# Optimization experiments

Hardware: AMD Instinct MI355X
Metric: run time of the kernel (lower is better)

Reference implementation:

```python
import jax, jax.numpy as jnp
import numpy as np

IN_F, OUT_F, K = 1024, 1024, 12
EPS = 1e-6


def setup_inputs() -> dict:
    key = jax.random.key(0)
    k1, k2, k3, k4 = jax.random.split(key, 4)
    x = jax.random.normal(k1, (4, 4096, IN_F), dtype=jnp.float32)
    # grid: linspace(-2,2,K) per feature + small noise so sort is nontrivial
    base = jnp.linspace(-2.0, 2.0, K, dtype=jnp.float32)
    grid = base[None, :] + 0.1 * jax.random.normal(k2, (IN_F, K), dtype=jnp.float32)
    coeffs = 0.1 * jax.random.normal(k3, (IN_F, K), dtype=jnp.float32)
    tangents = jnp.zeros((IN_F, K), dtype=jnp.float32)
    knot_alive = jnp.full((IN_F, K), 3.0, dtype=jnp.float32)
    kw1, kw2 = jax.random.split(k4)
    proj_w = jax.random.normal(kw1, (OUT_F, IN_F), dtype=jnp.float32) / np.sqrt(IN_F)
    proj_b = jnp.zeros((OUT_F,), dtype=jnp.float32)
    res_w = jax.random.normal(kw2, (OUT_F, IN_F), dtype=jnp.float32) / np.sqrt(IN_F)
    return {"x": x, "grid": grid, "coeffs": coeffs, "tangents": tangents,
            "knot_alive": knot_alive, "proj_w": proj_w, "proj_b": proj_b, "res_w": res_w}


def _eval_hermite_spline(x, grid, coeffs, tangents, knot_alive):
    # sort knots per input feature (grid: [F,K])
    sort_idx = jnp.argsort(grid, axis=1)
    sorted_grid = jnp.take_along_axis(grid, sort_idx, axis=1)
    sorted_coeffs = jnp.take_along_axis(coeffs, sort_idx, axis=1)
    sorted_tangents = jnp.take_along_axis(tangents, sort_idx, axis=1)
    sorted_alive = jnp.take_along_axis(knot_alive, sort_idx, axis=1)
    alive = jax.nn.sigmoid(sorted_alive)
    mc = sorted_coeffs * alive          # masked heights [F,K]
    mt = sorted_tangents * alive        # masked tangents [F,K]

    orig_shape = x.shape
    xf = x.reshape(-1, orig_shape[-1])  # [M,F]
    gmin = sorted_grid[:, 0]            # [F]
    gmax = sorted_grid[:, -1]
    xc = jnp.clip(xf, gmin[None, :], gmax[None, :])
    grange = jnp.maximum(gmax - gmin, EPS)
    xn = (xc - gmin[None, :]) / grange[None, :] * (K - 1)  # [M,F]
    idx_l = jnp.clip(xn.astype(jnp.int32), 0, K - 2)
    t = xn - idx_l.astype(xf.dtype)

    feat = jnp.arange(xf.shape[1])[None, :]  # [1,F] broadcast against [M,F] idx
    p0 = mc[feat, idx_l]
    p1 = mc[feat, idx_l + 1]
    m0 = mt[feat, idx_l]
    m1 = mt[feat, idx_l + 1]
    x_left = sorted_grid[feat, idx_l]
    x_right = sorted_grid[feat, idx_l + 1]
    dx = jnp.maximum(x_right - x_left, EPS)

    t2 = t * t
    t3 = t2 * t
    h00 = 2 * t3 - 3 * t2 + 1
    h10 = t3 - 2 * t2 + t
    h01 = -2 * t3 + 3 * t2
    h11 = t3 - t2
    out = h00 * p0 + h10 * m0 * dx + h01 * p1 + h11 * m1 * dx
    return out.reshape(orig_shape)


def reference(x, grid, coeffs, tangents, knot_alive, proj_w, proj_b, res_w):
    spline_out = _eval_hermite_spline(x, grid, coeffs, tangents, knot_alive)
    # proj(spline_out) + residual(x); torch Linear: y = x @ W.T + b
    return (jnp.einsum('...i,oi->...o', spline_out, proj_w) + proj_b
            + jnp.einsum('...i,oi->...o', x, res_w))
```

## Files before the change

kernel.cpp:

```cpp
#include <hip/hip_runtime.h>
#include <hip/hip_bf16.h>


#define IN_F   1024
#define OUT_F  1024
#define KNOTS  12
#define M_ROWS 16384
#define GK     2048

#define BM   256
#define BN   256
#define BKT  64
#define NTK  (GK / BKT)

typedef __attribute__((ext_vector_type(8))) __bf16 bf16x8;
typedef __attribute__((ext_vector_type(4))) float  f32x4;

__device__ __forceinline__ unsigned short f2bf(float v) {
    unsigned int u = __float_as_uint(v);
    u = (u + 0x7fffu + ((u >> 16) & 1u)) >> 16;
    return (unsigned short)u;
}

__device__ __forceinline__ void gload16(const void* g, void* l) {
    __builtin_amdgcn_global_load_lds(
        (const __attribute__((address_space(1))) void*)g,
        (__attribute__((address_space(3))) void*)l, 16, 0, 0);
}

__global__ __launch_bounds__(256) void prep_kernel(
    const float* __restrict__ grid, const float* __restrict__ coeffs,
    const float* __restrict__ tangents, const float* __restrict__ alive,
    float* __restrict__ gmin, float* __restrict__ scale, float4* __restrict__ H)
{
    int f = blockIdx.x * blockDim.x + threadIdx.x;
    if (f >= IN_F) return;
    float g[KNOTS], c[KNOTS], t[KNOTS], a[KNOTS];
    for (int i = 0; i < KNOTS; ++i) {
        g[i] = grid[f*KNOTS+i];  c[i] = coeffs[f*KNOTS+i];
        t[i] = tangents[f*KNOTS+i]; a[i] = alive[f*KNOTS+i];
    }
    for (int i = 1; i < KNOTS; ++i) {
        float gk=g[i], ck=c[i], tk=t[i], ak=a[i];
        int j = i-1;
        while (j >= 0 && g[j] > gk) { g[j+1]=g[j]; c[j+1]=c[j]; t[j+1]=t[j]; a[j+1]=a[j]; --j; }
        g[j+1]=gk; c[j+1]=ck; t[j+1]=tk; a[j+1]=ak;
    }
    float mcl[KNOTS], mtl[KNOTS];
    for (int i = 0; i < KNOTS; ++i) {
        float s = 1.f / (1.f + expf(-a[i]));
        mcl[i] = c[i]*s;  mtl[i] = t[i]*s;
    }
    gmin[f] = g[0];
    float grange = fmaxf(g[KNOTS-1] - g[0], 1e-6f);
    scale[f] = (float)(KNOTS-1) / grange;
    for (int k = 0; k < KNOTS-1; ++k) {
        float dx = fmaxf(g[k+1]-g[k], 1e-6f);
        H[(size_t)f*KNOTS + k] = make_float4(mcl[k], mcl[k+1], mtl[k]*dx, mtl[k+1]*dx);
    }
    H[(size_t)f*KNOTS + KNOTS-1] = make_float4(0.f, 0.f, 0.f, 0.f);
}

#define SROWS 64
#define HPAD  13
__global__ __launch_bounds__(256) void spline_kernel(const float* __restrict__ x,
    const float* __restrict__ gmin, const float* __restrict__ scale,
    const float4* __restrict__ H, unsigned short* __restrict__ A)
{
    __shared__ float4 sH[256 * HPAD];
    __shared__ float  sGm[256], sSc[256];
    const int tid  = threadIdx.x;
    const int fblk = blockIdx.y * 256;
    #pragma unroll
    for (int k = 0; k < KNOTS; ++k) sH[tid*HPAD + k] = H[(size_t)(fblk+tid)*KNOTS + k];
    sGm[tid] = gmin[fblk+tid];
    sSc[tid] = scale[fblk+tid];
    __syncthreads();

    const int wave = tid >> 6, lane = tid & 63;
    const int f0 = lane * 4;
    const float4 gm4 = *reinterpret_cast<const float4*>(&sGm[f0]);
    const float4 sc4 = *reinterpret_cast<const float4*>(&sSc[f0]);
    const float gms[4] = {gm4.x, gm4.y, gm4.z, gm4.w};
    const float scs[4] = {sc4.x, sc4.y, sc4.z, sc4.w};
    const int r0 = blockIdx.x * SROWS;

    #pragma unroll 2
    for (int r = wave; r < SROWS; r += 4) {
        const int row = r0 + r;
        const float4 xv = *reinterpret_cast<const float4*>(x + (size_t)row*IN_F + fblk + f0);
        const float xs[4] = {xv.x, xv.y, xv.z, xv.w};
        ushort4 so, xo;
        unsigned short* sp = (unsigned short*)&so;
        unsigned short* xp = (unsigned short*)&xo;
        #pragma unroll
        for (int j = 0; j < 4; ++j) {
            const float xi = xs[j];
            float xn = (xi - gms[j]) * scs[j];
            xn = fminf(fmaxf(xn, 0.f), (float)(KNOTS-1));
            int idx = (int)xn;  idx = idx > (KNOTS-2) ? (KNOTS-2) : idx;
            const float tt = xn - (float)idx;
            const float4 h = sH[(f0+j)*HPAD + idx];
            const float t2 = tt*tt, t3 = t2*tt;
            const float h00 =  2.f*t3 - 3.f*t2 + 1.f;
            const float h01 = -2.f*t3 + 3.f*t2;
            const float h10 =  t3 - 2.f*t2 + tt;
            const float h11 =  t3 - t2;
            sp[j] = f2bf(h00*h.x + h01*h.y + h10*h.z + h11*h.w);
            xp[j] = f2bf(xi);
        }
        const size_t base = (size_t)row * GK + fblk + f0;
        *reinterpret_cast<ushort4*>(A + base)        = so;
        *reinterpret_cast<ushort4*>(A + base + IN_F) = xo;
    }
}

__global__ __launch_bounds__(256) void bcast_kernel(
    const float* __restrict__ P, const float* __restrict__ R,
    unsigned short* __restrict__ Bc)
{
    int g = blockIdx.x*256 + threadIdx.x;
    int n  = g >> 9;
    int k4 = (g & 511) * 4;
    const float* src = (k4 < IN_F) ? (P + (size_t)n*IN_F + k4)
                                   : (R + (size_t)n*IN_F + (k4 - IN_F));
    float4 v = *reinterpret_cast<const float4*>(src);
    ushort4 o;
    o.x = f2bf(v.x); o.y = f2bf(v.y); o.z = f2bf(v.z); o.w = f2bf(v.w);
    *reinterpret_cast<ushort4*>(Bc + (size_t)n*GK + k4) = o;
}

__global__ __launch_bounds__(1024, 4) void gemm_kernel(
    const unsigned short* __restrict__ A, const unsigned short* __restrict__ B,
    const float* __restrict__ bias, float* __restrict__ C)
{
    __shared__ unsigned short sA[2][BM*BKT];
    __shared__ unsigned short sB[2][BN*BKT];

    const int tid  = threadIdx.x;
    const int wg   = blockIdx.x;
    const int swzb = (wg & 7) * 32 + (wg >> 3);
    const int by   = swzb >> 2;
    const int bx   = swzb & 3;

    const int lane = tid & 63;
    const int wave = tid >> 6;
    const int wm   = wave >> 2;
    const int wn   = wave & 3;
    const int lr   = lane & 15;
    const int lsl  = lane >> 4;

    const size_t aRow0 = (size_t)by * BM;
    const size_t bRow0 = (size_t)bx * BN;

    auto stage = [&](const unsigned short* __restrict__ G, size_t gRow0,
                     unsigned short* lds, int ts) {
        const int k0 = ts * BKT;
        #pragma unroll
        for (int i = 0; i < 2; ++i) {
            const int L16  = i*1024 + tid;
            const int lrow = L16 >> 3;
            const int ss   = (L16 & 7) ^ (lrow & 7);
            gload16(G + (gRow0 + lrow)*GK + k0 + ss*8, lds + (size_t)L16*8);
        }
    };
    auto rd = [&](const unsigned short* s, int lrow, int ks) -> bf16x8 {
        const int sp = (ks*4 + lsl) ^ (lrow & 7);
        return *reinterpret_cast<const bf16x8*>(s + lrow*BKT + sp*8);
    };

    f32x4 acc[4][4] = {};

    stage(A, aRow0, &sA[0][0], 0);
    stage(B, bRow0, &sB[0][0], 0);

    for (int t = 0; t < NTK; ++t) {
        const int b = t & 1;
        const unsigned short* cA = &sA[b][0];
        const unsigned short* cB = &sB[b][0];

        asm volatile("s_waitcnt vmcnt(0)" ::: "memory");
        __builtin_amdgcn_s_barrier();

        {
            bf16x8 av[4], bv[4];
            #pragma unroll
            for (int m = 0; m < 4; ++m) av[m] = rd(cA, wm*64 + m*16 + lr, 0);
            #pragma unroll
            for (int n = 0; n < 4; ++n) bv[n] = rd(cB, wn*64 + n*16 + lr, 0);
            if (t + 1 < NTK) {
                stage(A, aRow0, &sA[b^1][0], t+1);
                stage(B, bRow0, &sB[b^1][0], t+1);
            }
            __builtin_amdgcn_s_setprio(1);
            #pragma unroll
            for (int m = 0; m < 4; ++m)
              #pragma unroll
              for (int n = 0; n < 4; ++n)
                acc[m][n] = __builtin_amdgcn_mfma_f32_16x16x32_bf16(av[m], bv[n], acc[m][n], 0, 0, 0);
            __builtin_amdgcn_s_setprio(0);
        }
        {
            bf16x8 av[4], bv[4];
            #pragma unroll
            for (int m = 0; m < 4; ++m) av[m] = rd(cA, wm*64 + m*16 + lr, 1);
            #pragma unroll
            for (int n = 0; n < 4; ++n) bv[n] = rd(cB, wn*64 + n*16 + lr, 1);
            __builtin_amdgcn_s_setprio(1);
            #pragma unroll
            for (int m = 0; m < 4; ++m)
              #pragma unroll
              for (int n = 0; n < 4; ++n)
                acc[m][n] = __builtin_amdgcn_mfma_f32_16x16x32_bf16(av[m], bv[n], acc[m][n], 0, 0, 0);
            __builtin_amdgcn_s_setprio(0);
        }
    }

    #pragma unroll
    for (int n = 0; n < 4; ++n) {
        const int col = bx*BN + wn*64 + n*16 + lr;
        const float bv = bias[col];
        #pragma unroll
        for (int m = 0; m < 4; ++m) {
            const int grow = by*BM + wm*64 + m*16 + lsl*4;
            #pragma unroll
            for (int r = 0; r < 4; ++r)
                C[(size_t)(grow + r)*OUT_F + col] = acc[m][n][r] + bv;
        }
    }
}

__global__ __launch_bounds__(256) void fallback_kernel(
    const float* __restrict__ x, const float* __restrict__ P,
    const float* __restrict__ R, const float* __restrict__ pb,
    const float* __restrict__ gmin, const float* __restrict__ scale,
    const float4* __restrict__ H, float* __restrict__ out)
{
    __shared__ float s_s[IN_F];
    __shared__ float s_x[IN_F];
    int row = blockIdx.x;
    const float* xr = x + (size_t)row*IN_F;
    for (int f = threadIdx.x; f < IN_F; f += 256) {
        float xi = xr[f];
        float xn = (xi - gmin[f]) * scale[f];
        xn = fminf(fmaxf(xn, 0.f), (float)(KNOTS-1));
        int idx = (int)xn;  idx = idx > (KNOTS-2) ? (KNOTS-2) : idx;
        float tt = xn - (float)idx;
        float4 h = H[(size_t)f*KNOTS + idx];
        float t2 = tt*tt, t3 = t2*tt;
        s_s[f] = (2.f*t3-3.f*t2+1.f)*h.x + (-2.f*t3+3.f*t2)*h.y
               + (t3-2.f*t2+tt)*h.z + (t3-t2)*h.w;
        s_x[f] = xi;
    }
    __syncthreads();
    for (int j = 0; j < 4; ++j) {
        int o = threadIdx.x + j*256;
        const float* Pr = P + (size_t)o*IN_F;
        const float* Rr = R + (size_t)o*IN_F;
        float acc = pb[o];
        for (int f = 0; f < IN_F; ++f)
            acc = fmaf(s_s[f], Pr[f], fmaf(s_x[f], Rr[f], acc));
        out[(size_t)row*OUT_F + o] = acc;
    }
}

extern "C" void kernel_launch(void* const* d_in, const int* in_sizes, int n_in,
                              void* d_out, int out_size, void* d_ws, size_t ws_size,
                              hipStream_t stream) {
    const float* x         = (const float*)d_in[0];
    const float* grid      = (const float*)d_in[1];
    const float* coeffs    = (const float*)d_in[2];
    const float* tangents  = (const float*)d_in[3];
    const float* knotalive = (const float*)d_in[4];
    const float* proj_w    = (const float*)d_in[5];
    const float* proj_b    = (const float*)d_in[6];
    const float* res_w     = (const float*)d_in[7];
    float* out = (float*)d_out;

    const size_t needB  = (size_t)OUT_F * GK * 2;
    const size_t needA  = (size_t)M_ROWS * GK * 2;
    const size_t needT  = ((size_t)IN_F*2 + (size_t)IN_F*KNOTS*4) * 4;

    char* ws = (char*)d_ws;
    if (ws_size >= needB + needA + needT) {
        unsigned short* Bcat = (unsigned short*)ws;
        unsigned short* Abuf = (unsigned short*)(ws + needB);
        float*  gmin = (float*)(ws + needB + needA);
        float*  scl  = gmin + IN_F;
        float4* H    = (float4*)(scl + IN_F);

        prep_kernel<<<(IN_F+255)/256, 256, 0, stream>>>(grid, coeffs, tangents, knotalive,
                                                        gmin, scl, H);
        bcast_kernel<<<(OUT_F*GK/4)/256, 256, 0, stream>>>(proj_w, res_w, Bcat);
        spline_kernel<<<dim3(M_ROWS/SROWS, IN_F/256), 256, 0, stream>>>(x, gmin, scl, H, Abuf);
        gemm_kernel<<<(M_ROWS/BM)*(OUT_F/BN), 1024, 0, stream>>>(Abuf, Bcat, proj_b, out);
    } else {
        float*  gmin = (float*)ws;
        float*  scl  = gmin + IN_F;
        float4* H    = (float4*)(scl + IN_F);
        prep_kernel<<<(IN_F+255)/256, 256, 0, stream>>>(grid, coeffs, tangents, knotalive,
                                                        gmin, scl, H);
        fallback_kernel<<<M_ROWS, 256, 0, stream>>>(x, proj_w, res_w, proj_b,
                                                    gmin, scl, H, out);
    }
}
```

Baseline: 104.7 us.

## Switch GEMM to triple-buffered LDS pipeline with BK=32 and prefetch depth two

Halves the K tile to 32 and moves the GEMM from double to triple buffering. Loads are issued two steps ahead and the kernel waits on vmcnt(2) instead of draining all loads every step. The LDS swizzle is reworked for the 4-chunk row layout, and each thread now issues one global-to-LDS load per matrix per step. This hides more global latency, but doubles the number of barriers per K step and gives less MFMA work between them.

```diff
diff --git a/kernel.cpp b/kernel.cpp
--- a/kernel.cpp
+++ b/kernel.cpp
@@ -10,7 +10,7 @@
 
 #define BM   256
 #define BN   256
-#define BKT  64
+#define BKT  32
 #define NTK  (GK / BKT)
 
 typedef __attribute__((ext_vector_type(8))) __bf16 bf16x8;
@@ -134,8 +134,8 @@
     const unsigned short* __restrict__ A, const unsigned short* __restrict__ B,
     const float* __restrict__ bias, float* __restrict__ C)
 {
-    __shared__ unsigned short sA[2][BM*BKT];
-    __shared__ unsigned short sB[2][BN*BKT];
+    __shared__ unsigned short sA[3][BM*BKT];
+    __shared__ unsigned short sB[3][BN*BKT];
 
     const int tid  = threadIdx.x;
     const int wg   = blockIdx.x;
@@ -153,19 +153,15 @@
     const size_t aRow0 = (size_t)by * BM;
     const size_t bRow0 = (size_t)bx * BN;
 
+    const int srow = tid >> 2;
+    const int sq   = tid & 3;
+    const int ss   = sq ^ ((srow >> 1) & 3);
     auto stage = [&](const unsigned short* __restrict__ G, size_t gRow0,
                      unsigned short* lds, int ts) {
-        const int k0 = ts * BKT;
-        #pragma unroll
-        for (int i = 0; i < 2; ++i) {
-            const int L16  = i*1024 + tid;
-            const int lrow = L16 >> 3;
-            const int ss   = (L16 & 7) ^ (lrow & 7);
-            gload16(G + (gRow0 + lrow)*GK + k0 + ss*8, lds + (size_t)L16*8);
-        }
+        gload16(G + (gRow0 + srow)*GK + ts*BKT + ss*8, lds + (size_t)tid*8);
     };
-    auto rd = [&](const unsigned short* s, int lrow, int ks) -> bf16x8 {
-        const int sp = (ks*4 + lsl) ^ (lrow & 7);
+    auto rd = [&](const unsigned short* s, int lrow) -> bf16x8 {
+        const int sp = lsl ^ ((lrow >> 1) & 3);
         return *reinterpret_cast<const bf16x8*>(s + lrow*BKT + sp*8);
     };
 
@@ -173,47 +169,39 @@
 
     stage(A, aRow0, &sA[0][0], 0);
     stage(B, bRow0, &sB[0][0], 0);
-
+    stage(A, aRow0, &sA[1][0], 1);
+    stage(B, bRow0, &sB[1][0], 1);
+
+    int b = 0;
     for (int t = 0; t < NTK; ++t) {
-        const int b = t & 1;
         const unsigned short* cA = &sA[b][0];
         const unsigned short* cB = &sB[b][0];
 
-        asm volatile("s_waitcnt vmcnt(0)" ::: "memory");
+        if (t == NTK-1) asm volatile("s_waitcnt vmcnt(0)" ::: "memory");
+        else            asm volatile("s_waitcnt vmcnt(2)" ::: "memory");
         __builtin_amdgcn_s_barrier();
 
-        {
-            bf16x8 av[4], bv[4];
-            #pragma unroll
-            for (int m = 0; m < 4; ++m) av[m] = rd(cA, wm*64 + m*16 + lr, 0);
-            #pragma unroll
-            for (int n = 0; n < 4; ++n) bv[n] = rd(cB, wn*64 + n*16 + lr, 0);
-            if (t + 1 < NTK) {
-                stage(A, aRow0, &sA[b^1][0], t+1);
-                stage(B, bRow0, &sB[b^1][0], t+1);
-            }
-            __builtin_amdgcn_s_setprio(1);
-            #pragma unroll
-            for (int m = 0; m < 4; ++m)
-              #pragma unroll
-              for (int n = 0; n < 4; ++n)
-                acc[m][n] = __builtin_amdgcn_mfma_f32_16x16x32_bf16(av[m], bv[n], acc[m][n], 0, 0, 0);
-            __builtin_amdgcn_s_setprio(0);
+        bf16x8 av[4], bv[4];
+        #pragma unroll
+        for (int m = 0; m < 4; ++m) av[m] = rd(cA, wm*64 + m*16 + lr);
+        #pragma unroll
+        for (int n = 0; n < 4; ++n) bv[n] = rd(cB, wn*64 + n*16 + lr);
+
+        if (t + 2 < NTK) {
+            int b2 = b + 2; if (b2 >= 3) b2 -= 3;
+            stage(A, aRow0, &sA[b2][0], t+2);
+            stage(B, bRow0, &sB[b2][0], t+2);
         }
-        {
-            bf16x8 av[4], bv[4];
-            #pragma unroll
-            for (int m = 0; m < 4; ++m) av[m] = rd(cA, wm*64 + m*16 + lr, 1);
-            #pragma unroll
-            for (int n = 0; n < 4; ++n) bv[n] = rd(cB, wn*64 + n*16 + lr, 1);
-            __builtin_amdgcn_s_setprio(1);
-            #pragma unroll
-            for (int m = 0; m < 4; ++m)
-              #pragma unroll
-              for (int n = 0; n < 4; ++n)
-                acc[m][n] = __builtin_amdgcn_mfma_f32_16x16x32_bf16(av[m], bv[n], acc[m][n], 0, 0, 0);
-            __builtin_amdgcn_s_setprio(0);
-        }
+
+        __builtin_amdgcn_s_setprio(1);
+        #pragma unroll
+        for (int m = 0; m < 4; ++m)
+          #pragma unroll
+          for (int n = 0; n < 4; ++n)
+            acc[m][n] = __builtin_amdgcn_mfma_f32_16x16x32_bf16(av[m], bv[n], acc[m][n], 0, 0, 0);
+        __builtin_amdgcn_s_setprio(0);
+
+        ++b; if (b >= 3) b = 0;
     }
 
     #pragma unroll
```

Measured after the change: 107.0 us. +2.3%, slower.
